# Optimization experiments

Hardware: AMD Instinct MI355X
Metric: run time of the kernel (lower is better)

The kernel has to match this reference:

```python
import jax, jax.numpy as jnp
from jax import lax
import numpy as np

B, T, NX, NXS, NY, NYS, H = 4096, 60, 4, 3, 4, 3, 128


def lstm(x, h0, c0, Wih, Whh, bih, bhh):
    """PyTorch-convention LSTM. x: [B,T,D] -> (hs [B,T,H], hT, cT). Gate order i,f,g,o."""
    xg = jnp.einsum('btd,gd->btg', x, Wih) + bih  # [B,T,4H] precomputed input gates

    def step(carry, xg_t):
        h, c = carry
        g = xg_t + h @ Whh.T + bhh
        i, f, gg, o = jnp.split(g, 4, axis=-1)
        c = jax.nn.sigmoid(f) * c + jax.nn.sigmoid(i) * jnp.tanh(gg)
        h = jax.nn.sigmoid(o) * jnp.tanh(c)
        return (h, c), h

    (hT, cT), hs = lax.scan(step, (h0, c0), jnp.swapaxes(xg, 0, 1))
    return jnp.swapaxes(hs, 0, 1), hT, cT


def setup_inputs() -> dict:
    key = jax.random.key(0)
    ks = jax.random.split(key, 24)
    s = 0.1  # weight init scale
    inp = {
        'inputs_main': jax.random.normal(ks[0], (B, T, NX), jnp.float32),
        'inputs_sfc': jax.random.normal(ks[1], (B, NXS), jnp.float32),
        'rnn1_mem': jax.random.normal(ks[2], (B, T, H), jnp.float32),
        'hx2': jax.random.normal(ks[3], (B, H), jnp.float32),
        'cx2': jax.random.normal(ks[4], (B, H), jnp.float32),
        # surface MLPs -> initial h/c of rnn1
        'W_sfc1': s * jax.random.normal(ks[5], (H, NXS), jnp.float32),
        'b_sfc1': s * jax.random.normal(ks[6], (H,), jnp.float32),
        'W_sfc2': s * jax.random.normal(ks[7], (H, NXS), jnp.float32),
        'b_sfc2': s * jax.random.normal(ks[8], (H,), jnp.float32),
        # rnn1: input dim nx + nh_mem = 4 + 128 = 132
        'Wih1': s * jax.random.normal(ks[9], (4 * H, NX + H), jnp.float32),
        'Whh1': s * jax.random.normal(ks[10], (4 * H, H), jnp.float32),
        'bih1': s * jax.random.normal(ks[11], (4 * H,), jnp.float32),
        'bhh1': s * jax.random.normal(ks[12], (4 * H,), jnp.float32),
        # rnn2: input dim H
        'Wih2': s * jax.random.normal(ks[13], (4 * H, H), jnp.float32),
        'Whh2': s * jax.random.normal(ks[14], (4 * H, H), jnp.float32),
        'bih2': s * jax.random.normal(ks[15], (4 * H,), jnp.float32),
        'bhh2': s * jax.random.normal(ks[16], (4 * H,), jnp.float32),
        # intermediate + output MLPs
        'W_lat': s * jax.random.normal(ks[17], (H, H), jnp.float32),
        'b_lat': s * jax.random.normal(ks[18], (H,), jnp.float32),
        'W_out': s * jax.random.normal(ks[19], (NY, H), jnp.float32),
        'b_out': s * jax.random.normal(ks[20], (NY,), jnp.float32),
        'W_so': s * jax.random.normal(ks[21], (NYS, H), jnp.float32),
        'b_so': s * jax.random.normal(ks[22], (NYS,), jnp.float32),
    }
    return inp


def reference(inputs_main, inputs_sfc, rnn1_mem, hx2, cx2,
              W_sfc1, b_sfc1, W_sfc2, b_sfc2,
              Wih1, Whh1, bih1, bhh1,
              Wih2, Whh2, bih2, bhh2,
              W_lat, b_lat, W_out, b_out, W_so, b_so):
    # initial states of rnn1 from surface features
    hx = jnp.tanh(inputs_sfc @ W_sfc1.T + b_sfc1)
    cx = jnp.tanh(inputs_sfc @ W_sfc2.T + b_sfc2)
    # flip vertical levels, concat memory feedback
    x = jnp.flip(inputs_main, axis=1)
    x = jnp.concatenate([x, rnn1_mem], axis=2)  # [B,T,NX+H]
    rnn1out, _, _ = lstm(x, hx, cx, Wih1, Whh1, bih1, bhh1)
    rnn1out = jnp.flip(rnn1out, axis=1)
    # second LSTM over the opposite direction, random initial state
    rnn2out, last_h, _ = lstm(rnn1out, hx2, cx2, Wih2, Whh2, bih2, bhh2)
    # intermediate mlp (also becomes next-step memory in the stateful module)
    lat = rnn2out @ W_lat.T + b_lat  # [B,T,H]
    out = lat @ W_out.T + b_out      # [B,T,NY]
    out_sfc = last_h @ W_so.T + b_so  # [B,NYS]
    return out, out_sfc
```

## Files before the change

kernel.cpp:

```cpp
#include <hip/hip_runtime.h>
#include <stdint.h>


typedef __bf16 bf16x8 __attribute__((ext_vector_type(8)));
typedef __bf16 bf16x4 __attribute__((ext_vector_type(4)));
typedef float  f32x4  __attribute__((ext_vector_type(4)));

#define H0_OFF  0u
#define X0_OFF  8192u
#define XA_OFF  16384u
#define LDS_SZ  24576

__device__ __forceinline__ bf16x8 ldw8(const float* __restrict__ p){
  float4 a = *(const float4*)p;
  float4 b = *(const float4*)(p+4);
  bf16x8 r;
  r[0]=(__bf16)a.x; r[1]=(__bf16)a.y; r[2]=(__bf16)a.z; r[3]=(__bf16)a.w;
  r[4]=(__bf16)b.x; r[5]=(__bf16)b.y; r[6]=(__bf16)b.z; r[7]=(__bf16)b.w;
  return r;
}
__device__ __forceinline__ void load_wgate(bf16x8 (&dst)[8], const float* pih, const float* phh, int gg){
  #pragma unroll
  for (int kk=0;kk<4;++kk) dst[kk]   = ldw8(pih + kk*32 + gg*8);
  #pragma unroll
  for (int kk=0;kk<4;++kk) dst[4+kk] = ldw8(phh + kk*32 + gg*8);
}
__device__ __forceinline__ void step_barrier(){
  asm volatile("s_waitcnt lgkmcnt(0)\n\ts_barrier" ::: "memory");
}
__device__ __forceinline__ void lstm_pw(const f32x4& a0, const f32x4& a1,
                                        const f32x4& a2, const f32x4& a3,
                                        float (&c_)[4], float (&hn)[4]){
  #pragma unroll
  for (int i=0;i<4;++i){
    float ei = __expf(-a0[i]);
    float ef = __expf(-a1[i]);
    float eg = __expf(-2.0f*__builtin_fabsf(a2[i]));
    float sf = __builtin_amdgcn_rcpf(1.0f + ef);
    float itg = __builtin_copysignf((1.0f-eg)*__builtin_amdgcn_rcpf((1.0f+ei)*(1.0f+eg)), a2[i]);
    float ci = sf*c_[i] + itg;
    float eo = __expf(-a3[i]);
    float ec = __expf(-2.0f*__builtin_fabsf(ci));
    c_[i] = ci;
    hn[i] = __builtin_copysignf((1.0f-ec)*__builtin_amdgcn_rcpf((1.0f+eo)*(1.0f+ec)), ci);
  }
}

__global__ void comb_kernel(const float* __restrict__ W_lat, const float* __restrict__ b_lat,
                            const float* __restrict__ W_out, const float* __restrict__ b_out,
                            float* __restrict__ wcomb){
  int tid = threadIdx.x;
  int m = tid >> 7, k = tid & 127;
  float s = 0.f;
  for (int a=0;a<128;++a) s += W_out[m*128+a]*W_lat[a*128+k];
  wcomb[tid] = s;
  if (tid < 4){
    float sb = b_out[tid];
    for (int a=0;a<128;++a) sb += W_out[tid*128+a]*b_lat[a];
    wcomb[512+tid] = sb;
  }
}

#define MFMA4(BASE, K0) \
  { _Pragma("unroll") \
    for (int kk=0;kk<4;++kk){ \
      uint4 q = *(const uint4*)(lds + (BASE) + ((abase + 64u*(uint32_t)kk) ^ amask)); \
      bf16x8 af = __builtin_bit_cast(bf16x8, q); \
      a0 = __builtin_amdgcn_mfma_f32_16x16x32_bf16(af, wB0[kk+(K0)], a0, 0,0,0); \
      a1 = __builtin_amdgcn_mfma_f32_16x16x32_bf16(af, wB1[kk+(K0)], a1, 0,0,0); \
      a2 = __builtin_amdgcn_mfma_f32_16x16x32_bf16(af, wB2[kk+(K0)], a2, 0,0,0); \
      a3 = __builtin_amdgcn_mfma_f32_16x16x32_bf16(af, wB3[kk+(K0)], a3, 0,0,0); \
    } }

#define MFMA4_OUT(BASE, K0) \
  { _Pragma("unroll") \
    for (int kk=0;kk<4;++kk){ \
      uint4 q = *(const uint4*)(lds + (BASE) + ((abase + 64u*(uint32_t)kk) ^ amask)); \
      bf16x8 af = __builtin_bit_cast(bf16x8, q); \
      a0 = __builtin_amdgcn_mfma_f32_16x16x32_bf16(af, wB0[kk+(K0)], a0, 0,0,0); \
      a1 = __builtin_amdgcn_mfma_f32_16x16x32_bf16(af, wB1[kk+(K0)], a1, 0,0,0); \
      a2 = __builtin_amdgcn_mfma_f32_16x16x32_bf16(af, wB2[kk+(K0)], a2, 0,0,0); \
      a3 = __builtin_amdgcn_mfma_f32_16x16x32_bf16(af, wB3[kk+(K0)], a3, 0,0,0); \
      ao = __builtin_amdgcn_mfma_f32_16x16x32_bf16(af, wcB[kk], ao, 0,0,0); \
    } }

__global__ __launch_bounds__(512, 2)
void lstm_fused(const float* __restrict__ xmain_g, const float* __restrict__ sfc,
                const float* __restrict__ mem_g, const float* __restrict__ hx2g,
                const float* __restrict__ cx2g,
                const float* __restrict__ Wsfc1, const float* __restrict__ bsfc1,
                const float* __restrict__ Wsfc2, const float* __restrict__ bsfc2,
                const float* __restrict__ Wih1, const float* __restrict__ Whh1,
                const float* __restrict__ bih1, const float* __restrict__ bhh1,
                const float* __restrict__ Wih2, const float* __restrict__ Whh2,
                const float* __restrict__ bih2, const float* __restrict__ bhh2,
                const float* __restrict__ Wso, const float* __restrict__ bso,
                const float* __restrict__ wcomb_ws,
                uint2* __restrict__ ws_u2, float* __restrict__ dout)
{
  __shared__ __align__(16) unsigned char lds[LDS_SZ];
  const int tid = threadIdx.x;
  const int w   = tid >> 6;
  const int l   = tid & 63;
  const int gg  = l >> 4;
  const int l16 = l & 15;
  const int blk = blockIdx.x;
  const int b0  = blk * 16;
  const int j   = (w<<4) + l16;
  const uint32_t amask = (uint32_t)((l16 & 7) << 4);
  const uint32_t abase = (uint32_t)(l16*256 + gg*16);
  const int srow = tid >> 5;
  const uint32_t stg_off = (uint32_t)(((srow*256) + (tid&31)*8) ^ ((srow&7)<<4));
  uint32_t hw_off[4];
  #pragma unroll
  for (int i=0;i<4;++i){
    int r = gg*4 + i;
    hw_off[i] = (uint32_t)((r*256 + j*2) ^ ((r&7)<<4));
  }
  const size_t ws_base = (size_t)blk * 60 * 512;

  #pragma unroll
  for (int e = tid; e < 960; e += 512){
    int t = e >> 4, row = e & 15;
    float4 xv = *(const float4*)(xmain_g + (size_t)(b0+row)*240 + t*4);
    bf16x4 b4; b4[0]=(__bf16)xv.x; b4[1]=(__bf16)xv.y; b4[2]=(__bf16)xv.z; b4[3]=(__bf16)xv.w;
    *(bf16x4*)(lds + XA_OFF + (uint32_t)e*8u) = b4;
  }
  const float* memrow = mem_g + (size_t)(b0 + srow)*7680 + (tid&31)*4;
  {
    float4 mv = *(const float4*)memrow;
    bf16x4 m4; m4[0]=(__bf16)mv.x; m4[1]=(__bf16)mv.y; m4[2]=(__bf16)mv.z; m4[3]=(__bf16)mv.w;
    *(bf16x4*)(lds + X0_OFF + stg_off) = m4;
  }
  {
    int c0 = (tid&31)*4;
    float4 wa = *(const float4*)(Wsfc1 + c0*3);
    float4 wb = *(const float4*)(Wsfc1 + c0*3 + 4);
    float4 wc = *(const float4*)(Wsfc1 + c0*3 + 8);
    const float* sp = sfc + (size_t)(b0+srow)*3;
    float s0 = sp[0], s1 = sp[1], s2 = sp[2];
    float4 bb = *(const float4*)(bsfc1 + c0);
    float v0 = tanhf(bb.x + s0*wa.x + s1*wa.y + s2*wa.z);
    float v1 = tanhf(bb.y + s0*wa.w + s1*wb.x + s2*wb.y);
    float v2 = tanhf(bb.z + s0*wb.z + s1*wb.w + s2*wc.x);
    float v3 = tanhf(bb.w + s0*wc.y + s1*wc.z + s2*wc.w);
    bf16x4 h4; h4[0]=(__bf16)v0; h4[1]=(__bf16)v1; h4[2]=(__bf16)v2; h4[3]=(__bf16)v3;
    *(bf16x4*)(lds + H0_OFF + stg_off) = h4;
  }
  float c_[4];
  {
    const float* wr = Wsfc2 + j*3;
    float w0_=wr[0], w1_=wr[1], w2_=wr[2];
    float bj = bsfc2[j];
    #pragma unroll
    for (int i=0;i<4;++i){
      const float* sp = sfc + (size_t)(b0 + gg*4 + i)*3;
      c_[i] = tanhf(bj + sp[0]*w0_ + sp[1]*w1_ + sp[2]*w2_);
    }
  }
  bf16x8 wB0[8], wB1[8], wB2[8], wB3[8];
  load_wgate(wB0, Wih1 + 4 + (size_t)(0*128+j)*132, Whh1 + (size_t)(0*128+j)*128, gg);
  load_wgate(wB1, Wih1 + 4 + (size_t)(1*128+j)*132, Whh1 + (size_t)(1*128+j)*128, gg);
  load_wgate(wB2, Wih1 + 4 + (size_t)(2*128+j)*132, Whh1 + (size_t)(2*128+j)*128, gg);
  load_wgate(wB3, Wih1 + 4 + (size_t)(3*128+j)*132, Whh1 + (size_t)(3*128+j)*128, gg);
  bf16x8 wxB0 = {}, wxB1 = {}, wxB2 = {}, wxB3 = {};
  if (gg == 0){
    float4 x0 = *(const float4*)(Wih1 + (size_t)(0*128+j)*132);
    float4 x1 = *(const float4*)(Wih1 + (size_t)(1*128+j)*132);
    float4 x2 = *(const float4*)(Wih1 + (size_t)(2*128+j)*132);
    float4 x3 = *(const float4*)(Wih1 + (size_t)(3*128+j)*132);
    wxB0[0]=(__bf16)x0.x; wxB0[1]=(__bf16)x0.y; wxB0[2]=(__bf16)x0.z; wxB0[3]=(__bf16)x0.w;
    wxB1[0]=(__bf16)x1.x; wxB1[1]=(__bf16)x1.y; wxB1[2]=(__bf16)x1.z; wxB1[3]=(__bf16)x1.w;
    wxB2[0]=(__bf16)x2.x; wxB2[1]=(__bf16)x2.y; wxB2[2]=(__bf16)x2.z; wxB2[3]=(__bf16)x2.w;
    wxB3[0]=(__bf16)x3.x; wxB3[1]=(__bf16)x3.y; wxB3[2]=(__bf16)x3.z; wxB3[3]=(__bf16)x3.w;
  }
  float bias0 = bih1[0*128+j] + bhh1[0*128+j];
  float bias1 = bih1[1*128+j] + bhh1[1*128+j];
  float bias2 = bih1[2*128+j] + bhh1[2*128+j];
  float bias3 = bih1[3*128+j] + bhh1[3*128+j];
  float4 P0 = *(const float4*)(memrow + 128);
  step_barrier();

  #pragma unroll 1
  for (int t=0; t<60; ++t){
    const uint32_t cur = (uint32_t)(t & 1), nxt = cur ^ 1u;
    const uint32_t Hc = H0_OFF + cur*4096u, Xc = X0_OFF + cur*4096u;
    float4 P1;
    if (t+2 < 60) P1 = *(const float4*)(memrow + (size_t)(t+2)*128);
    if (t > 0){
      uint2 hv = *(const uint2*)(lds + Hc + stg_off);
      ws_u2[ws_base + (size_t)(t-1)*512 + tid] = hv;
    }
    const int tt = 59 - t;
    bf16x8 xa = {};
    if (gg == 0){
      bf16x4 x4 = *(const bf16x4*)(lds + XA_OFF + (uint32_t)((tt<<4) + l16)*8u);
      xa[0]=x4[0]; xa[1]=x4[1]; xa[2]=x4[2]; xa[3]=x4[3];
    }
    f32x4 a0 = {bias0,bias0,bias0,bias0};
    f32x4 a1 = {bias1,bias1,bias1,bias1};
    f32x4 a2 = {bias2,bias2,bias2,bias2};
    f32x4 a3 = {bias3,bias3,bias3,bias3};
    a0 = __builtin_amdgcn_mfma_f32_16x16x32_bf16(xa, wxB0, a0, 0,0,0);
    a1 = __builtin_amdgcn_mfma_f32_16x16x32_bf16(xa, wxB1, a1, 0,0,0);
    a2 = __builtin_amdgcn_mfma_f32_16x16x32_bf16(xa, wxB2, a2, 0,0,0);
    a3 = __builtin_amdgcn_mfma_f32_16x16x32_bf16(xa, wxB3, a3, 0,0,0);
    MFMA4(Xc, 0)
    MFMA4(Hc, 4)
    float hn[4];
    lstm_pw(a0, a1, a2, a3, c_, hn);
    if (t < 59){
      bf16x4 m4; m4[0]=(__bf16)P0.x; m4[1]=(__bf16)P0.y; m4[2]=(__bf16)P0.z; m4[3]=(__bf16)P0.w;
      *(bf16x4*)(lds + X0_OFF + nxt*4096u + stg_off) = m4;
    }
    #pragma unroll
    for (int i=0;i<4;++i)
      *(__bf16*)(lds + H0_OFF + nxt*4096u + hw_off[i]) = (__bf16)hn[i];
    P0 = P1;
    step_barrier();
  }
  { uint2 hv = *(const uint2*)(lds + H0_OFF + stg_off);
    ws_u2[ws_base + (size_t)59*512 + tid] = hv; }
  ((uint2*)(lds + X0_OFF))[tid] = ((const uint2*)(lds + H0_OFF))[tid];
  step_barrier();

  {
    float4 hv = *(const float4*)(hx2g + (size_t)(b0+srow)*128 + (tid&31)*4);
    bf16x4 h4; h4[0]=(__bf16)hv.x; h4[1]=(__bf16)hv.y; h4[2]=(__bf16)hv.z; h4[3]=(__bf16)hv.w;
    *(bf16x4*)(lds + H0_OFF + stg_off) = h4;
  }
  #pragma unroll
  for (int i=0;i<4;++i) c_[i] = cx2g[(size_t)(b0 + gg*4 + i)*128 + j];
  load_wgate(wB0, Wih2 + (size_t)(0*128+j)*128, Whh2 + (size_t)(0*128+j)*128, gg);
  load_wgate(wB1, Wih2 + (size_t)(1*128+j)*128, Whh2 + (size_t)(1*128+j)*128, gg);
  load_wgate(wB2, Wih2 + (size_t)(2*128+j)*128, Whh2 + (size_t)(2*128+j)*128, gg);
  load_wgate(wB3, Wih2 + (size_t)(3*128+j)*128, Whh2 + (size_t)(3*128+j)*128, gg);
  bias0 = bih2[0*128+j] + bhh2[0*128+j];
  bias1 = bih2[1*128+j] + bhh2[1*128+j];
  bias2 = bih2[2*128+j] + bhh2[2*128+j];
  bias3 = bih2[3*128+j] + bhh2[3*128+j];
  bf16x8 wcB[4];
  #pragma unroll
  for (int kk=0;kk<4;++kk){
    bf16x8 v = {};
    if (l16 < 4) v = ldw8(wcomb_ws + l16*128 + kk*32 + gg*8);
    wcB[kk] = v;
  }
  const float bc = (l16 < 4) ? wcomb_ws[512 + l16] : 0.f;
  asm volatile("s_waitcnt vmcnt(0) lgkmcnt(0)" ::: "memory");
  __builtin_amdgcn_s_barrier();
  uint2 P0u = ws_u2[ws_base + (size_t)58*512 + tid];

  #pragma unroll 1
  for (int t=0; t<60; ++t){
    const uint32_t cur = (uint32_t)(t & 1), nxt = cur ^ 1u;
    const uint32_t Hc = H0_OFF + cur*4096u, Xc = X0_OFF + cur*4096u;
    uint2 P1u;
    if (t+2 < 60) P1u = ws_u2[ws_base + (size_t)(57-t)*512 + tid];
    f32x4 a0 = {bias0,bias0,bias0,bias0};
    f32x4 a1 = {bias1,bias1,bias1,bias1};
    f32x4 a2 = {bias2,bias2,bias2,bias2};
    f32x4 a3 = {bias3,bias3,bias3,bias3};
    f32x4 ao = {0.f,0.f,0.f,0.f};
    MFMA4(Xc, 0)
    MFMA4_OUT(Hc, 4)
    float hn[4];
    lstm_pw(a0, a1, a2, a3, c_, hn);
    if (t > 0 && w == 0 && l16 < 4){
      #pragma unroll
      for (int i=0;i<4;++i)
        dout[(size_t)(b0 + gg*4 + i)*240 + (size_t)(t-1)*4 + l16] = ao[i] + bc;
    }
    if (t < 59)
      *(uint2*)(lds + X0_OFF + nxt*4096u + stg_off) = P0u;
    #pragma unroll
    for (int i=0;i<4;++i)
      *(__bf16*)(lds + H0_OFF + nxt*4096u + hw_off[i]) = (__bf16)hn[i];
    P0u = P1u;
    step_barrier();
  }

  {
    bf16x8 wsB[4];
    #pragma unroll
    for (int kk=0;kk<4;++kk){
      bf16x8 v = {};
      if (l16 < 3) v = ldw8(Wso + l16*128 + kk*32 + gg*8);
      wsB[kk] = v;
    }
    f32x4 ao = {0.f,0.f,0.f,0.f};
    f32x4 as_ = {0.f,0.f,0.f,0.f};
    #pragma unroll
    for (int kk=0;kk<4;++kk){
      uint4 q = *(const uint4*)(lds + H0_OFF + ((abase + 64u*(uint32_t)kk) ^ amask));
      bf16x8 af = __builtin_bit_cast(bf16x8, q);
      ao  = __builtin_amdgcn_mfma_f32_16x16x32_bf16(af, wcB[kk], ao, 0,0,0);
      as_ = __builtin_amdgcn_mfma_f32_16x16x32_bf16(af, wsB[kk], as_, 0,0,0);
    }
    if (w == 0 && l16 < 4){
      #pragma unroll
      for (int i=0;i<4;++i)
        dout[(size_t)(b0 + gg*4 + i)*240 + 59*4 + l16] = ao[i] + bc;
    }
    if (w == 0 && l16 < 3){
      float bs = bso[l16];
      #pragma unroll
      for (int i=0;i<4;++i)
        dout[983040 + (size_t)(b0 + gg*4 + i)*3 + l16] = as_[i] + bs;
    }
  }
}

extern "C" void kernel_launch(void* const* d_in, const int* in_sizes, int n_in,
                              void* d_out, int out_size, void* d_ws, size_t ws_size,
                              hipStream_t stream){
  const float* inputs_main = (const float*)d_in[0];
  const float* inputs_sfc  = (const float*)d_in[1];
  const float* rnn1_mem    = (const float*)d_in[2];
  const float* hx2  = (const float*)d_in[3];
  const float* cx2  = (const float*)d_in[4];
  const float* W_sfc1 = (const float*)d_in[5];
  const float* b_sfc1 = (const float*)d_in[6];
  const float* W_sfc2 = (const float*)d_in[7];
  const float* b_sfc2 = (const float*)d_in[8];
  const float* Wih1 = (const float*)d_in[9];
  const float* Whh1 = (const float*)d_in[10];
  const float* bih1 = (const float*)d_in[11];
  const float* bhh1 = (const float*)d_in[12];
  const float* Wih2 = (const float*)d_in[13];
  const float* Whh2 = (const float*)d_in[14];
  const float* bih2 = (const float*)d_in[15];
  const float* bhh2 = (const float*)d_in[16];
  const float* W_lat = (const float*)d_in[17];
  const float* b_lat = (const float*)d_in[18];
  const float* W_out = (const float*)d_in[19];
  const float* b_out = (const float*)d_in[20];
  const float* W_so  = (const float*)d_in[21];
  const float* b_so  = (const float*)d_in[22];
  float* out = (float*)d_out;
  uint2* ws_u2 = (uint2*)d_ws;
  float* wcomb = (float*)((char*)d_ws + 62914560u);

  comb_kernel<<<dim3(1), dim3(512), 0, stream>>>(W_lat, b_lat, W_out, b_out, wcomb);
  lstm_fused<<<dim3(256), dim3(512), 0, stream>>>(inputs_main, inputs_sfc, rnn1_mem, hx2, cx2,
      W_sfc1, b_sfc1, W_sfc2, b_sfc2, Wih1, Whh1, bih1, bhh1, Wih2, Whh2, bih2, bhh2,
      W_so, b_so, wcomb, ws_u2, out);
}
```

Baseline: 209.4 us.

## Keep most rnn1 hidden states in LDS and prescale gate weights for exp2

LDS grows to about 160 KB so that the last 34 rnn1 hidden states stay on-chip as a history buffer. Only the first 26 timesteps still round-trip through the global workspace, which cuts global writes and reads between the two LSTM passes. Gate weights and biases are pre-multiplied by -log2(e) (or -2·log2(e) for the g gate), so the activations can call exp2 directly without a per-step negate or scale; the sign/abs handling for the g gate is replaced by a clamp. The combined output-projection MFMA now runs only in wave 0. The large LDS footprint limits each CU to one block, and the clamp-based tanh form may behave differently for extreme gate values.

After: 194.2 us (median of 2 runs). 1.08x faster.

```diff
diff --git a/kernel.cpp b/kernel.cpp
--- a/kernel.cpp
+++ b/kernel.cpp
@@ -6,24 +6,30 @@
 typedef __bf16 bf16x4 __attribute__((ext_vector_type(4)));
 typedef float  f32x4  __attribute__((ext_vector_type(4)));
 
+#define HQ      4096u
 #define H0_OFF  0u
-#define X0_OFF  8192u
+#define XD_OFF  8192u
 #define XA_OFF  16384u
-#define LDS_SZ  24576
-
-__device__ __forceinline__ bf16x8 ldw8(const float* __restrict__ p){
+#define HIST    24064u
+#define LDS_SZ  163328
+#define NWS     26
+
+#define S1f (-1.4426950408889634f)
+#define S2f (-2.8853900817779268f)
+
+__device__ __forceinline__ bf16x8 ldw8s(const float* __restrict__ p, float s){
   float4 a = *(const float4*)p;
   float4 b = *(const float4*)(p+4);
   bf16x8 r;
-  r[0]=(__bf16)a.x; r[1]=(__bf16)a.y; r[2]=(__bf16)a.z; r[3]=(__bf16)a.w;
-  r[4]=(__bf16)b.x; r[5]=(__bf16)b.y; r[6]=(__bf16)b.z; r[7]=(__bf16)b.w;
+  r[0]=(__bf16)(a.x*s); r[1]=(__bf16)(a.y*s); r[2]=(__bf16)(a.z*s); r[3]=(__bf16)(a.w*s);
+  r[4]=(__bf16)(b.x*s); r[5]=(__bf16)(b.y*s); r[6]=(__bf16)(b.z*s); r[7]=(__bf16)(b.w*s);
   return r;
 }
-__device__ __forceinline__ void load_wgate(bf16x8 (&dst)[8], const float* pih, const float* phh, int gg){
-  #pragma unroll
-  for (int kk=0;kk<4;++kk) dst[kk]   = ldw8(pih + kk*32 + gg*8);
-  #pragma unroll
-  for (int kk=0;kk<4;++kk) dst[4+kk] = ldw8(phh + kk*32 + gg*8);
+__device__ __forceinline__ void load_wgate(bf16x8 (&dst)[8], const float* pih, const float* phh, int gg, float s){
+  #pragma unroll
+  for (int kk=0;kk<4;++kk) dst[kk]   = ldw8s(pih + kk*32 + gg*8, s);
+  #pragma unroll
+  for (int kk=0;kk<4;++kk) dst[4+kk] = ldw8s(phh + kk*32 + gg*8, s);
 }
 __device__ __forceinline__ void step_barrier(){
   asm volatile("s_waitcnt lgkmcnt(0)\n\ts_barrier" ::: "memory");
@@ -33,16 +39,17 @@
                                         float (&c_)[4], float (&hn)[4]){
   #pragma unroll
   for (int i=0;i<4;++i){
-    float ei = __expf(-a0[i]);
-    float ef = __expf(-a1[i]);
-    float eg = __expf(-2.0f*__builtin_fabsf(a2[i]));
+    float ei = __builtin_amdgcn_exp2f(a0[i]);
+    float ef = __builtin_amdgcn_exp2f(a1[i]);
+    float eg = __builtin_amdgcn_exp2f(fminf(a2[i], 126.0f));
+    float eo = __builtin_amdgcn_exp2f(a3[i]);
     float sf = __builtin_amdgcn_rcpf(1.0f + ef);
-    float itg = __builtin_copysignf((1.0f-eg)*__builtin_amdgcn_rcpf((1.0f+ei)*(1.0f+eg)), a2[i]);
+    float itg = (1.0f - eg) * __builtin_amdgcn_rcpf((1.0f + ei)*(1.0f + eg));
     float ci = sf*c_[i] + itg;
-    float eo = __expf(-a3[i]);
-    float ec = __expf(-2.0f*__builtin_fabsf(ci));
+    float ec = __builtin_amdgcn_exp2f(S2f*__builtin_fabsf(ci));
+    float th = (1.0f - ec) * __builtin_amdgcn_rcpf((1.0f + eo)*(1.0f + ec));
     c_[i] = ci;
-    hn[i] = __builtin_copysignf((1.0f-ec)*__builtin_amdgcn_rcpf((1.0f+eo)*(1.0f+ec)), ci);
+    hn[i] = __builtin_copysignf(th, ci);
   }
 }
 
@@ -70,18 +77,6 @@
       a1 = __builtin_amdgcn_mfma_f32_16x16x32_bf16(af, wB1[kk+(K0)], a1, 0,0,0); \
       a2 = __builtin_amdgcn_mfma_f32_16x16x32_bf16(af, wB2[kk+(K0)], a2, 0,0,0); \
       a3 = __builtin_amdgcn_mfma_f32_16x16x32_bf16(af, wB3[kk+(K0)], a3, 0,0,0); \
-    } }
-
-#define MFMA4_OUT(BASE, K0) \
-  { _Pragma("unroll") \
-    for (int kk=0;kk<4;++kk){ \
-      uint4 q = *(const uint4*)(lds + (BASE) + ((abase + 64u*(uint32_t)kk) ^ amask)); \
-      bf16x8 af = __builtin_bit_cast(bf16x8, q); \
-      a0 = __builtin_amdgcn_mfma_f32_16x16x32_bf16(af, wB0[kk+(K0)], a0, 0,0,0); \
-      a1 = __builtin_amdgcn_mfma_f32_16x16x32_bf16(af, wB1[kk+(K0)], a1, 0,0,0); \
-      a2 = __builtin_amdgcn_mfma_f32_16x16x32_bf16(af, wB2[kk+(K0)], a2, 0,0,0); \
-      a3 = __builtin_amdgcn_mfma_f32_16x16x32_bf16(af, wB3[kk+(K0)], a3, 0,0,0); \
-      ao = __builtin_amdgcn_mfma_f32_16x16x32_bf16(af, wcB[kk], ao, 0,0,0); \
     } }
 
 __global__ __launch_bounds__(512, 2)
@@ -117,7 +112,7 @@
     int r = gg*4 + i;
     hw_off[i] = (uint32_t)((r*256 + j*2) ^ ((r&7)<<4));
   }
-  const size_t ws_base = (size_t)blk * 60 * 512;
+  const size_t ws_base = (size_t)blk * NWS * 512;
 
   #pragma unroll
   for (int e = tid; e < 960; e += 512){
@@ -130,7 +125,7 @@
   {
     float4 mv = *(const float4*)memrow;
     bf16x4 m4; m4[0]=(__bf16)mv.x; m4[1]=(__bf16)mv.y; m4[2]=(__bf16)mv.z; m4[3]=(__bf16)mv.w;
-    *(bf16x4*)(lds + X0_OFF + stg_off) = m4;
+    *(bf16x4*)(lds + XD_OFF + stg_off) = m4;
   }
   {
     int c0 = (tid&31)*4;
@@ -159,37 +154,39 @@
     }
   }
   bf16x8 wB0[8], wB1[8], wB2[8], wB3[8];
-  load_wgate(wB0, Wih1 + 4 + (size_t)(0*128+j)*132, Whh1 + (size_t)(0*128+j)*128, gg);
-  load_wgate(wB1, Wih1 + 4 + (size_t)(1*128+j)*132, Whh1 + (size_t)(1*128+j)*128, gg);
-  load_wgate(wB2, Wih1 + 4 + (size_t)(2*128+j)*132, Whh1 + (size_t)(2*128+j)*128, gg);
-  load_wgate(wB3, Wih1 + 4 + (size_t)(3*128+j)*132, Whh1 + (size_t)(3*128+j)*128, gg);
+  load_wgate(wB0, Wih1 + 4 + (size_t)(0*128+j)*132, Whh1 + (size_t)(0*128+j)*128, gg, S1f);
+  load_wgate(wB1, Wih1 + 4 + (size_t)(1*128+j)*132, Whh1 + (size_t)(1*128+j)*128, gg, S1f);
+  load_wgate(wB2, Wih1 + 4 + (size_t)(2*128+j)*132, Whh1 + (size_t)(2*128+j)*128, gg, S2f);
+  load_wgate(wB3, Wih1 + 4 + (size_t)(3*128+j)*132, Whh1 + (size_t)(3*128+j)*128, gg, S1f);
   bf16x8 wxB0 = {}, wxB1 = {}, wxB2 = {}, wxB3 = {};
   if (gg == 0){
     float4 x0 = *(const float4*)(Wih1 + (size_t)(0*128+j)*132);
     float4 x1 = *(const float4*)(Wih1 + (size_t)(1*128+j)*132);
     float4 x2 = *(const float4*)(Wih1 + (size_t)(2*128+j)*132);
     float4 x3 = *(const float4*)(Wih1 + (size_t)(3*128+j)*132);
-    wxB0[0]=(__bf16)x0.x; wxB0[1]=(__bf16)x0.y; wxB0[2]=(__bf16)x0.z; wxB0[3]=(__bf16)x0.w;
-    wxB1[0]=(__bf16)x1.x; wxB1[1]=(__bf16)x1.y; wxB1[2]=(__bf16)x1.z; wxB1[3]=(__bf16)x1.w;
-    wxB2[0]=(__bf16)x2.x; wxB2[1]=(__bf16)x2.y; wxB2[2]=(__bf16)x2.z; wxB2[3]=(__bf16)x2.w;
-    wxB3[0]=(__bf16)x3.x; wxB3[1]=(__bf16)x3.y; wxB3[2]=(__bf16)x3.z; wxB3[3]=(__bf16)x3.w;
-  }
-  float bias0 = bih1[0*128+j] + bhh1[0*128+j];
-  float bias1 = bih1[1*128+j] + bhh1[1*128+j];
-  float bias2 = bih1[2*128+j] + bhh1[2*128+j];
-  float bias3 = bih1[3*128+j] + bhh1[3*128+j];
+    wxB0[0]=(__bf16)(x0.x*S1f); wxB0[1]=(__bf16)(x0.y*S1f); wxB0[2]=(__bf16)(x0.z*S1f); wxB0[3]=(__bf16)(x0.w*S1f);
+    wxB1[0]=(__bf16)(x1.x*S1f); wxB1[1]=(__bf16)(x1.y*S1f); wxB1[2]=(__bf16)(x1.z*S1f); wxB1[3]=(__bf16)(x1.w*S1f);
+    wxB2[0]=(__bf16)(x2.x*S2f); wxB2[1]=(__bf16)(x2.y*S2f); wxB2[2]=(__bf16)(x2.z*S2f); wxB2[3]=(__bf16)(x2.w*S2f);
+    wxB3[0]=(__bf16)(x3.x*S1f); wxB3[1]=(__bf16)(x3.y*S1f); wxB3[2]=(__bf16)(x3.z*S1f); wxB3[3]=(__bf16)(x3.w*S1f);
+  }
+  float bias0 = (bih1[0*128+j] + bhh1[0*128+j])*S1f;
+  float bias1 = (bih1[1*128+j] + bhh1[1*128+j])*S1f;
+  float bias2 = (bih1[2*128+j] + bhh1[2*128+j])*S2f;
+  float bias3 = (bih1[3*128+j] + bhh1[3*128+j])*S1f;
   float4 P0 = *(const float4*)(memrow + 128);
   step_barrier();
 
   #pragma unroll 1
   for (int t=0; t<60; ++t){
     const uint32_t cur = (uint32_t)(t & 1), nxt = cur ^ 1u;
-    const uint32_t Hc = H0_OFF + cur*4096u, Xc = X0_OFF + cur*4096u;
+    const uint32_t Hc = H0_OFF + cur*HQ;
+    const uint32_t xbase = (t >= NWS) ? (HIST + (uint32_t)(t-NWS)*HQ) : (XD_OFF + cur*HQ);
     float4 P1;
     if (t+2 < 60) P1 = *(const float4*)(memrow + (size_t)(t+2)*128);
     if (t > 0){
       uint2 hv = *(const uint2*)(lds + Hc + stg_off);
-      ws_u2[ws_base + (size_t)(t-1)*512 + tid] = hv;
+      if (t <= NWS) ws_u2[ws_base + (size_t)(t-1)*512 + tid] = hv;
+      else *(uint2*)(lds + HIST + (uint32_t)(t-1-NWS)*HQ + stg_off) = hv;
     }
     const int tt = 59 - t;
     bf16x8 xa = {};
@@ -205,65 +202,84 @@
     a1 = __builtin_amdgcn_mfma_f32_16x16x32_bf16(xa, wxB1, a1, 0,0,0);
     a2 = __builtin_amdgcn_mfma_f32_16x16x32_bf16(xa, wxB2, a2, 0,0,0);
     a3 = __builtin_amdgcn_mfma_f32_16x16x32_bf16(xa, wxB3, a3, 0,0,0);
-    MFMA4(Xc, 0)
+    MFMA4(xbase, 0)
     MFMA4(Hc, 4)
     float hn[4];
     lstm_pw(a0, a1, a2, a3, c_, hn);
     if (t < 59){
+      const uint32_t sdst = (t+1 >= NWS) ? (HIST + (uint32_t)(t+1-NWS)*HQ) : (XD_OFF + nxt*HQ);
       bf16x4 m4; m4[0]=(__bf16)P0.x; m4[1]=(__bf16)P0.y; m4[2]=(__bf16)P0.z; m4[3]=(__bf16)P0.w;
-      *(bf16x4*)(lds + X0_OFF + nxt*4096u + stg_off) = m4;
+      *(bf16x4*)(lds + sdst + stg_off) = m4;
     }
     #pragma unroll
     for (int i=0;i<4;++i)
-      *(__bf16*)(lds + H0_OFF + nxt*4096u + hw_off[i]) = (__bf16)hn[i];
+      *(__bf16*)(lds + H0_OFF + nxt*HQ + hw_off[i]) = (__bf16)hn[i];
     P0 = P1;
     step_barrier();
   }
-  { uint2 hv = *(const uint2*)(lds + H0_OFF + stg_off);
-    ws_u2[ws_base + (size_t)59*512 + tid] = hv; }
-  ((uint2*)(lds + X0_OFF))[tid] = ((const uint2*)(lds + H0_OFF))[tid];
-  step_barrier();
-
   {
-    float4 hv = *(const float4*)(hx2g + (size_t)(b0+srow)*128 + (tid&31)*4);
-    bf16x4 h4; h4[0]=(__bf16)hv.x; h4[1]=(__bf16)hv.y; h4[2]=(__bf16)hv.z; h4[3]=(__bf16)hv.w;
+    uint2 hv = *(const uint2*)(lds + H0_OFF + stg_off);
+    *(uint2*)(lds + HIST + 33u*HQ + stg_off) = hv;
+    float4 h2v = *(const float4*)(hx2g + (size_t)(b0+srow)*128 + (tid&31)*4);
+    bf16x4 h4; h4[0]=(__bf16)h2v.x; h4[1]=(__bf16)h2v.y; h4[2]=(__bf16)h2v.z; h4[3]=(__bf16)h2v.w;
     *(bf16x4*)(lds + H0_OFF + stg_off) = h4;
   }
   #pragma unroll
   for (int i=0;i<4;++i) c_[i] = cx2g[(size_t)(b0 + gg*4 + i)*128 + j];
-  load_wgate(wB0, Wih2 + (size_t)(0*128+j)*128, Whh2 + (size_t)(0*128+j)*128, gg);
-  load_wgate(wB1, Wih2 + (size_t)(1*128+j)*128, Whh2 + (size_t)(1*128+j)*128, gg);
-  load_wgate(wB2, Wih2 + (size_t)(2*128+j)*128, Whh2 + (size_t)(2*128+j)*128, gg);
-  load_wgate(wB3, Wih2 + (size_t)(3*128+j)*128, Whh2 + (size_t)(3*128+j)*128, gg);
-  bias0 = bih2[0*128+j] + bhh2[0*128+j];
-  bias1 = bih2[1*128+j] + bhh2[1*128+j];
-  bias2 = bih2[2*128+j] + bhh2[2*128+j];
-  bias3 = bih2[3*128+j] + bhh2[3*128+j];
-  bf16x8 wcB[4];
-  #pragma unroll
-  for (int kk=0;kk<4;++kk){
-    bf16x8 v = {};
-    if (l16 < 4) v = ldw8(wcomb_ws + l16*128 + kk*32 + gg*8);
-    wcB[kk] = v;
+  load_wgate(wB0, Wih2 + (size_t)(0*128+j)*128, Whh2 + (size_t)(0*128+j)*128, gg, S1f);
+  load_wgate(wB1, Wih2 + (size_t)(1*128+j)*128, Whh2 + (size_t)(1*128+j)*128, gg, S1f);
+  load_wgate(wB2, Wih2 + (size_t)(2*128+j)*128, Whh2 + (size_t)(2*128+j)*128, gg, S2f);
+  load_wgate(wB3, Wih2 + (size_t)(3*128+j)*128, Whh2 + (size_t)(3*128+j)*128, gg, S1f);
+  float nb0 = (bih2[0*128+j] + bhh2[0*128+j])*S1f;
+  float nb1 = (bih2[1*128+j] + bhh2[1*128+j])*S1f;
+  float nb2 = (bih2[2*128+j] + bhh2[2*128+j])*S2f;
+  float nb3 = (bih2[3*128+j] + bhh2[3*128+j])*S1f;
+  bias0=nb0; bias1=nb1; bias2=nb2; bias3=nb3;
+  bf16x8 wcB[4] = {};
+  if (w == 0){
+    #pragma unroll
+    for (int kk=0;kk<4;++kk){
+      bf16x8 v = {};
+      if (l16 < 4) v = ldw8s(wcomb_ws + l16*128 + kk*32 + gg*8, 1.0f);
+      wcB[kk] = v;
+    }
   }
   const float bc = (l16 < 4) ? wcomb_ws[512 + l16] : 0.f;
   asm volatile("s_waitcnt vmcnt(0) lgkmcnt(0)" ::: "memory");
   __builtin_amdgcn_s_barrier();
-  uint2 P0u = ws_u2[ws_base + (size_t)58*512 + tid];
-
+
+  uint2 P0u, P1u;
   #pragma unroll 1
   for (int t=0; t<60; ++t){
     const uint32_t cur = (uint32_t)(t & 1), nxt = cur ^ 1u;
-    const uint32_t Hc = H0_OFF + cur*4096u, Xc = X0_OFF + cur*4096u;
-    uint2 P1u;
-    if (t+2 < 60) P1u = ws_u2[ws_base + (size_t)(57-t)*512 + tid];
+    const uint32_t Hc = H0_OFF + cur*HQ;
+    const int s = 59 - t;
+    const uint32_t xbase = (s >= NWS) ? (HIST + (uint32_t)(s-NWS)*HQ) : (XD_OFF + cur*HQ);
+    if (t >= 32 && t < 58) P1u = ws_u2[ws_base + (size_t)(57-t)*512 + tid];
     f32x4 a0 = {bias0,bias0,bias0,bias0};
     f32x4 a1 = {bias1,bias1,bias1,bias1};
     f32x4 a2 = {bias2,bias2,bias2,bias2};
     f32x4 a3 = {bias3,bias3,bias3,bias3};
     f32x4 ao = {0.f,0.f,0.f,0.f};
-    MFMA4(Xc, 0)
-    MFMA4_OUT(Hc, 4)
+    MFMA4(xbase, 0)
+    bf16x8 hf[4];
+    #pragma unroll
+    for (int kk=0;kk<4;++kk){
+      uint4 q = *(const uint4*)(lds + Hc + ((abase + 64u*(uint32_t)kk) ^ amask));
+      hf[kk] = __builtin_bit_cast(bf16x8, q);
+    }
+    #pragma unroll
+    for (int kk=0;kk<4;++kk){
+      a0 = __builtin_amdgcn_mfma_f32_16x16x32_bf16(hf[kk], wB0[kk+4], a0, 0,0,0);
+      a1 = __builtin_amdgcn_mfma_f32_16x16x32_bf16(hf[kk], wB1[kk+4], a1, 0,0,0);
+      a2 = __builtin_amdgcn_mfma_f32_16x16x32_bf16(hf[kk], wB2[kk+4], a2, 0,0,0);
+      a3 = __builtin_amdgcn_mfma_f32_16x16x32_bf16(hf[kk], wB3[kk+4], a3, 0,0,0);
+    }
+    if (w == 0){
+      #pragma unroll
+      for (int kk=0;kk<4;++kk)
+        ao = __builtin_amdgcn_mfma_f32_16x16x32_bf16(hf[kk], wcB[kk], ao, 0,0,0);
+    }
     float hn[4];
     lstm_pw(a0, a1, a2, a3, c_, hn);
     if (t > 0 && w == 0 && l16 < 4){
@@ -271,21 +287,21 @@
       for (int i=0;i<4;++i)
         dout[(size_t)(b0 + gg*4 + i)*240 + (size_t)(t-1)*4 + l16] = ao[i] + bc;
     }
-    if (t < 59)
-      *(uint2*)(lds + X0_OFF + nxt*4096u + stg_off) = P0u;
+    if (t >= 33 && t < 59)
+      *(uint2*)(lds + XD_OFF + nxt*HQ + stg_off) = P0u;
     #pragma unroll
     for (int i=0;i<4;++i)
-      *(__bf16*)(lds + H0_OFF + nxt*4096u + hw_off[i]) = (__bf16)hn[i];
+      *(__bf16*)(lds + H0_OFF + nxt*HQ + hw_off[i]) = (__bf16)hn[i];
     P0u = P1u;
     step_barrier();
   }
 
-  {
+  if (w == 0){
     bf16x8 wsB[4];
     #pragma unroll
     for (int kk=0;kk<4;++kk){
       bf16x8 v = {};
-      if (l16 < 3) v = ldw8(Wso + l16*128 + kk*32 + gg*8);
+      if (l16 < 3) v = ldw8s(Wso + l16*128 + kk*32 + gg*8, 1.0f);
       wsB[kk] = v;
     }
     f32x4 ao = {0.f,0.f,0.f,0.f};
@@ -297,12 +313,12 @@
       ao  = __builtin_amdgcn_mfma_f32_16x16x32_bf16(af, wcB[kk], ao, 0,0,0);
       as_ = __builtin_amdgcn_mfma_f32_16x16x32_bf16(af, wsB[kk], as_, 0,0,0);
     }
-    if (w == 0 && l16 < 4){
+    if (l16 < 4){
       #pragma unroll
       for (int i=0;i<4;++i)
         dout[(size_t)(b0 + gg*4 + i)*240 + 59*4 + l16] = ao[i] + bc;
     }
-    if (w == 0 && l16 < 3){
+    if (l16 < 3){
       float bs = bso[l16];
       #pragma unroll
       for (int i=0;i<4;++i)
```
